# Kernel tuning notes

Measured on AMD Instinct MI355X. Metric: run time of the kernel, lower is better.

The kernel has to match this reference:

```python
import jax, jax.numpy as jnp
import numpy as np

D_MODEL = 768
D_STATE = 64
EXPAND = 2
D_INNER = EXPAND * D_MODEL
B, L = 2, 1024


def setup_inputs() -> dict:
    key = jax.random.key(0)
    ks = jax.random.split(key, 12)
    def xavier(k, shape):
        fan_in, fan_out = shape[0], shape[1]
        a = np.sqrt(6.0 / (fan_in + fan_out)).astype(np.float32)
        return jax.random.uniform(k, shape, jnp.float32, -a, a)
    x = jax.random.normal(ks[0], (B, L, D_MODEL), jnp.float32)
    W_in = xavier(ks[1], (D_MODEL, 2 * D_INNER))
    W_x = xavier(ks[2], (D_INNER, 2 * D_STATE + D_INNER))
    W_dt = xavier(ks[3], (D_STATE, D_INNER))
    b_dt = jax.random.uniform(ks[4], (D_INNER,), jnp.float32, -0.1, 0.1)
    A_log = jax.random.uniform(ks[5], (D_INNER, D_STATE), jnp.float32, -4.0, -1.0)
    Dp = 1.0 + 0.1 * jax.random.normal(ks[6], (D_INNER,), jnp.float32)
    W_out = xavier(ks[7], (D_INNER, D_MODEL))
    ln_g = jnp.ones((D_MODEL,), jnp.float32)
    ln_b = jnp.zeros((D_MODEL,), jnp.float32)
    return {"x": x, "W_in": W_in, "W_x": W_x, "W_dt": W_dt, "b_dt": b_dt,
            "A_log": A_log, "Dp": Dp, "W_out": W_out, "ln_g": ln_g, "ln_b": ln_b}


def _s6_forward(x, W_in, W_x, W_dt, b_dt, A_log, Dp, W_out, ln_g, ln_b):
    residual = x
    xr = x @ W_in                                    # (B,L,2*d_inner)
    xs, res = xr[..., :D_INNER], xr[..., D_INNER:]
    xs = jax.nn.silu(xs)
    # selective scan parameters
    x_dbl = xs @ W_x                                 # (B,L,2*d_state+d_inner)
    B_sel = x_dbl[..., :D_STATE]                     # (B,L,d_state)
    delta_in = x_dbl[..., D_STATE:2 * D_STATE]       # (B,L,d_state)
    C_sel = x_dbl[..., 2 * D_STATE:]                 # (B,L,d_inner)
    delta = jax.nn.softplus(delta_in @ W_dt + b_dt)  # (B,L,d_inner)
    delta = jnp.minimum(delta, 10.0)
    A = -jnp.exp(A_log.astype(jnp.float32))          # (d_inner,d_state)

    def step(h, inp):
        x_t, d_t, B_t, C_t = inp                     # (B,di) (B,di) (B,ds) (B,di)
        dA = jnp.exp(d_t[:, :, None] * A[None])      # (B,di,ds)
        dB = d_t[:, :, None] * B_t[:, None, :]       # (B,di,ds)
        h = dA * h + dB * x_t[:, :, None]
        y_t = C_t * jnp.sum(h, axis=-1)              # (B,di): sum(C[...,None]*h,-1)
        return h, y_t

    h0 = jnp.zeros((x.shape[0], D_INNER, D_STATE), xs.dtype)
    time_major = lambda a: jnp.swapaxes(a, 0, 1)
    _, ys = jax.lax.scan(step, h0, (time_major(xs), time_major(delta),
                                    time_major(B_sel), time_major(C_sel)))
    y = jnp.swapaxes(ys, 0, 1)                       # (B,L,d_inner)
    y = y + xs * Dp
    y = y * jax.nn.silu(res)
    out = y @ W_out + residual
    mu = jnp.mean(out, axis=-1, keepdims=True)
    var = jnp.var(out, axis=-1, keepdims=True)
    return (out - mu) * jax.lax.rsqrt(var + 1e-5) * ln_g + ln_b


def reference(x, W_in, W_x, W_dt, b_dt, A_log, Dp, W_out, ln_g, ln_b):
    return _s6_forward(x, W_in, W_x, W_dt, b_dt, A_log, Dp, W_out, ln_g, ln_b)
```

## Files before the change

kernel.cpp:

```cpp
#include <hip/hip_runtime.h>

typedef __bf16 bf16x8 __attribute__((ext_vector_type(8)));
typedef short short8 __attribute__((ext_vector_type(8)));
typedef float f32x4 __attribute__((ext_vector_type(4)));
typedef unsigned short ushort_t;

__device__ __forceinline__ ushort_t f2bf(float f) {
  union { float f; unsigned u; } v; v.f = f;
  unsigned r = v.u + 0x7fffu + ((v.u >> 16) & 1u);
  return (ushort_t)(r >> 16);
}
__device__ __forceinline__ float bf2f(ushort_t u) {
  return __int_as_float(((unsigned)u) << 16);
}

__device__ __forceinline__ void g2lds16(const void* g, void* l) {
  __builtin_amdgcn_global_load_lds(
      (const __attribute__((address_space(1))) void*)g,
      (__attribute__((address_space(3))) void*)l, 16, 0, 0);
}

__device__ __forceinline__ float rlane(float v, int l) {
  return __int_as_float(__builtin_amdgcn_readlane(__float_as_int(v), l));
}

__device__ __forceinline__ float fexp2(float x) {
#if __has_builtin(__builtin_amdgcn_exp2f)
  return __builtin_amdgcn_exp2f(x);
#else
  return exp2f(x);
#endif
}

template<int CTRL>
__device__ __forceinline__ float dpp_step(float x) {
  int t = __builtin_amdgcn_update_dpp(0, __float_as_int(x), CTRL, 0xf, 0xf, false);
  return x + __int_as_float(t);
}
__device__ __forceinline__ float wave_sum64(float v) {
  v = dpp_step<0x111>(v);
  v = dpp_step<0x112>(v);
  v = dpp_step<0x114>(v);
  v = dpp_step<0x118>(v);
  v = dpp_step<0x142>(v);
  v = dpp_step<0x143>(v);
  return v;
}
__device__ __forceinline__ float row_sum16(float v) {
  v = dpp_step<0x111>(v);
  v = dpp_step<0x112>(v);
  v = dpp_step<0x114>(v);
  v = dpp_step<0x118>(v);
  return v;
}
__device__ __forceinline__ float bcast_row15(float v) {
  return __int_as_float(__builtin_amdgcn_ds_swizzle(__float_as_int(v), 0x1F0));
}

__global__ __launch_bounds__(256)
void prep_kernel(const float* __restrict__ x, ushort_t* __restrict__ xbf,
                 const float* __restrict__ W_in, ushort_t* __restrict__ WinT,
                 const float* __restrict__ W_x, ushort_t* __restrict__ WxT,
                 const float* __restrict__ W_out, ushort_t* __restrict__ WoutT) {
  __shared__ float tile[32][33];
  const int r = blockIdx.x, tid = threadIdx.x;
  if (r < 1536) {
    int i = (r * 256 + tid) * 4;
    float4 v = *(const float4*)(x + i);
    union { ushort_t u[4]; uint2 v2; } o;
    o.u[0] = f2bf(v.x); o.u[1] = f2bf(v.y); o.u[2] = f2bf(v.z); o.u[3] = f2bf(v.w);
    *(uint2*)(xbf + i) = o.v2;
    return;
  }
  const float* W; ushort_t* Wt; int K, N, bx, by;
  if (r < 3840)      { int rr = r - 1536; W = W_in;  Wt = WinT;  K = 768;  N = 3072; bx = rr % 96; by = rr / 96; }
  else if (r < 6336) { int rr = r - 3840; W = W_x;   Wt = WxT;   K = 1536; N = 1664; bx = rr % 52; by = rr / 52; }
  else               { int rr = r - 6336; W = W_out; Wt = WoutT; K = 1536; N = 768;  bx = rr % 24; by = rr / 24; }
  const int n0 = bx * 32, k0 = by * 32;
  const int tx = tid & 31, ty = tid >> 5;
#pragma unroll
  for (int rr = 0; rr < 32; rr += 8)
    tile[ty + rr][tx] = W[(size_t)(k0 + ty + rr) * N + n0 + tx];
  __syncthreads();
#pragma unroll
  for (int rr = 0; rr < 32; rr += 8)
    Wt[(size_t)(n0 + ty + rr) * K + k0 + tx] = f2bf(tile[tx][ty + rr]);
}

template<int MODE>
__global__ __launch_bounds__(256)
void gemm_bf16(const ushort_t* __restrict__ A, const ushort_t* __restrict__ Bt,
               const int K, float* __restrict__ out0, ushort_t* __restrict__ out1,
               float* __restrict__ out2, const float* __restrict__ resid) {
  __shared__ __align__(16) ushort_t Asl[128 * 32];
  __shared__ __align__(16) ushort_t Bsl[128 * 32];
  const int tid = threadIdx.x;
  const int lane = tid & 63;
  const int wid = tid >> 6;
  const int wm = wid >> 1, wn = wid & 1;
  const int lr = lane & 15, lk = lane >> 4;
  const int bm = blockIdx.y, bn = blockIdx.x;
  const ushort_t* Ab = A + (size_t)bm * 128 * K;
  const ushort_t* Bb = Bt + (size_t)bn * 128 * K;

  f32x4 acc[4][4];
#pragma unroll
  for (int i = 0; i < 4; ++i)
#pragma unroll
    for (int j = 0; j < 4; ++j) acc[i][j] = (f32x4){0.f, 0.f, 0.f, 0.f};

  for (int k0 = 0; k0 < K; k0 += 32) {
#pragma unroll
    for (int it = 0; it < 2; ++it) {
      const int cb = ((it << 2) + wid) << 6;
      const int ch = cb + lane;
      const int row = ch >> 2;
      const int c8 = (ch & 3) << 3;
      g2lds16(Ab + (size_t)row * K + k0 + c8, Asl + (size_t)cb * 8);
      g2lds16(Bb + (size_t)row * K + k0 + c8, Bsl + (size_t)cb * 8);
    }
    __syncthreads();
    short8 av[4], bv[4];
#pragma unroll
    for (int i = 0; i < 4; ++i)
      av[i] = *(const short8*)(Asl + ((wm * 64 + i * 16 + lr) * 32 + lk * 8));
#pragma unroll
    for (int j = 0; j < 4; ++j)
      bv[j] = *(const short8*)(Bsl + ((wn * 64 + j * 16 + lr) * 32 + lk * 8));
#pragma unroll
    for (int i = 0; i < 4; ++i)
#pragma unroll
      for (int j = 0; j < 4; ++j)
        acc[i][j] = __builtin_amdgcn_mfma_f32_16x16x32_bf16(
            __builtin_bit_cast(bf16x8, av[i]), __builtin_bit_cast(bf16x8, bv[j]),
            acc[i][j], 0, 0, 0);
    __syncthreads();
  }

  const int mb = bm * 128 + wm * 64 + (lane >> 4) * 4;
  const int nb = bn * 128 + wn * 64 + (lane & 15);
#pragma unroll
  for (int i = 0; i < 4; ++i) {
#pragma unroll
    for (int j = 0; j < 4; ++j) {
      const int n = nb + j * 16;
#pragma unroll
      for (int r = 0; r < 4; ++r) {
        const int m = mb + i * 16 + r;
        float v = acc[i][j][r];
        if (MODE == 0) {
          float sv = v / (1.f + __expf(-v));
          if (n < 1536) {
            out0[(size_t)m * 1536 + n] = sv;
            out1[(size_t)m * 1536 + n] = f2bf(sv);
          } else {
            out2[(size_t)m * 1536 + (n - 1536)] = sv;
          }
        } else if (MODE == 1) {
          out0[(size_t)m * 1664 + n] = v;
        } else {
          const size_t id = (size_t)m * 768 + n;
          out0[id] = v + resid[id];
        }
      }
    }
  }
}

__global__ __launch_bounds__(256)
void dt_gemm(const float* __restrict__ xdbl, const float* __restrict__ Wdt,
             const float* __restrict__ bdt, float* __restrict__ delta) {
  __shared__ float Wl[64][256];
  __shared__ float Xl[32][64];
  const int tid = threadIdx.x;
  const int n0 = blockIdx.x << 8;
  const int m0 = blockIdx.y << 5;
  for (int i = tid; i < 64 * 256; i += 256) {
    int k = i >> 8, nn = i & 255;
    Wl[k][nn] = Wdt[(size_t)k * 1536 + n0 + nn];
  }
  for (int i = tid; i < 32 * 64; i += 256) {
    int mm = i >> 6, k = i & 63;
    Xl[mm][k] = xdbl[(size_t)(m0 + mm) * 1664 + 64 + k];
  }
  __syncthreads();
  float bv = bdt[n0 + tid];
  for (int mm = 0; mm < 32; ++mm) {
    float acc = bv;
#pragma unroll
    for (int k = 0; k < 64; ++k) acc = fmaf(Xl[mm][k], Wl[k][tid], acc);
    float sp = fmaxf(acc, 0.f) + log1pf(__expf(-fabsf(acc)));
    delta[(size_t)(m0 + mm) * 1536 + n0 + tid] = fminf(sp, 10.f);
  }
}


__global__ __launch_bounds__(256, 4)
void scan_pass1(const float* __restrict__ xdbl, const float* __restrict__ delta,
                const float* __restrict__ xs, const float* __restrict__ A_log,
                float* __restrict__ Qb, float* __restrict__ Dsum) {
  __shared__ __align__(16) ushort_t Btl[64 * 64];
  __shared__ __align__(16) float2 dtdx[64][16];
  const int tid = threadIdx.x;
  const int lane = tid & 63;
  const int wid = tid >> 6;
  const int i16 = lane & 15;
  const int ch = wid * 4 + (lane >> 4);
  const int seg = blockIdx.x, b = blockIdx.z;
  const int d0 = blockIdx.y * 16;
  const int d = d0 + ch;
  const int t0 = seg << 6;
  const size_t r0 = (size_t)b * 1024;

#pragma unroll
  for (int i = 0; i < 4; ++i) {
    int q = i * 256 + tid;
    int t = q >> 4, s0 = (q & 15) << 2;
    float4 v = *(const float4*)(xdbl + (r0 + t0 + t) * 1664 + s0);
    ushort4 u;
    u.x = f2bf(v.x); u.y = f2bf(v.y); u.z = f2bf(v.z); u.w = f2bf(v.w);
    *(ushort4*)&Btl[t * 64 + s0] = u;
  }
  float dtg[4];
#pragma unroll
  for (int c = 0; c < 4; ++c) {
    int dc = d0 + wid * 4 + c;
    dtg[c] = delta[(r0 + t0 + lane) * 1536 + dc];
    float dxg = dtg[c] * xs[(r0 + t0 + lane) * 1536 + dc];
    dtdx[lane][(wid * 4 + c) ^ i16] = make_float2(dtg[c], dxg);
  }
  float ds0 = rlane(wave_sum64(dtg[0]), 63);
  float ds1 = rlane(wave_sum64(dtg[1]), 63);
  float ds2 = rlane(wave_sum64(dtg[2]), 63);
  float ds3 = rlane(wave_sum64(dtg[3]), 63);
  if (lane == 0) {
    const size_t sb0 = (size_t)(b * 16 + seg) * 1536 + d0 + wid * 4;
    *(float4*)(Dsum + sb0) = make_float4(ds0, ds1, ds2, ds3);
  }

  float4 Av = *(const float4*)(A_log + (size_t)d * 64 + i16 * 4);
  const float A0 = -__expf(Av.x) * 1.44269504f;
  const float A1 = -__expf(Av.y) * 1.44269504f;
  const float A2 = -__expf(Av.z) * 1.44269504f;
  const float A3 = -__expf(Av.w) * 1.44269504f;

  __syncthreads();

  const ushort_t* Brow = Btl + (i16 << 2);
  float h0 = 0.f, h1 = 0.f, h2 = 0.f, h3 = 0.f;
#pragma unroll
  for (int tt = 0; tt < 64; ++tt) {
    float2 dd = dtdx[tt][ch ^ (tt & 15)];
    ushort4 ub = *(const ushort4*)(Brow + tt * 64);
    float dA0 = fexp2(dd.x * A0), dA1 = fexp2(dd.x * A1);
    float dA2 = fexp2(dd.x * A2), dA3 = fexp2(dd.x * A3);
    h0 = fmaf(dA0, h0, dd.y * bf2f(ub.x));
    h1 = fmaf(dA1, h1, dd.y * bf2f(ub.y));
    h2 = fmaf(dA2, h2, dd.y * bf2f(ub.z));
    h3 = fmaf(dA3, h3, dd.y * bf2f(ub.w));
  }
  const size_t sb = (size_t)(b * 16 + seg) * 1536 + d;
  *(float4*)(Qb + sb * 64 + i16 * 4) = make_float4(h0, h1, h2, h3);
}

__global__ __launch_bounds__(256, 4)
void scan_combine(float* __restrict__ Qb, const float* __restrict__ Dsum,
                  const float* __restrict__ A_log) {
  const int tid = threadIdx.x;
  const int lane = tid & 63;
  const int wave = blockIdx.x * 4 + (tid >> 6);
  const int bb = (wave >= 1536) ? 1 : 0;
  const int d = wave - bb * 1536;
  const float Aval2 = -__expf(A_log[(size_t)d * 64 + lane]) * 1.44269504f;
  float h = 0.f;
#pragma unroll
  for (int j = 0; j < 16; ++j) {
    const size_t sb = ((size_t)(bb * 16 + j) * 1536 + d);
    float q = Qb[sb * 64 + lane];
    float P = fexp2(Aval2 * Dsum[sb]);
    Qb[sb * 64 + lane] = h;
    h = fmaf(P, h, q);
  }
}

__global__ __launch_bounds__(256, 4)
void scan_pass2(const float* __restrict__ xdbl, const float* __restrict__ delta,
                const float* __restrict__ xs, const float* __restrict__ sres,
                const float* __restrict__ A_log, const float* __restrict__ Dp,
                const float* __restrict__ Qb, ushort_t* __restrict__ ybf) {
  __shared__ __align__(16) ushort_t Btl[64 * 64];
  __shared__ __align__(16) float2 dtdx[64][16];
  __shared__ __align__(16) float ytmp[64][16];
  const int tid = threadIdx.x;
  const int lane = tid & 63;
  const int wid = tid >> 6;
  const int i16 = lane & 15;
  const int ch = wid * 4 + (lane >> 4);
  const int seg = blockIdx.x, b = blockIdx.z;
  const int d0 = blockIdx.y * 16;
  const int d = d0 + ch;
  const int t0 = seg << 6;
  const size_t r0 = (size_t)b * 1024;

#pragma unroll
  for (int i = 0; i < 4; ++i) {
    int q = i * 256 + tid;
    int t = q >> 4, s0 = (q & 15) << 2;
    float4 v = *(const float4*)(xdbl + (r0 + t0 + t) * 1664 + s0);
    ushort4 u;
    u.x = f2bf(v.x); u.y = f2bf(v.y); u.z = f2bf(v.z); u.w = f2bf(v.w);
    *(ushort4*)&Btl[t * 64 + s0] = u;
  }
#pragma unroll
  for (int c = 0; c < 4; ++c) {
    int dc = d0 + wid * 4 + c;
    float dt = delta[(r0 + t0 + lane) * 1536 + dc];
    float dx = dt * xs[(r0 + t0 + lane) * 1536 + dc];
    dtdx[lane][(wid * 4 + c) ^ i16] = make_float2(dt, dx);
  }

  float4 Av = *(const float4*)(A_log + (size_t)d * 64 + i16 * 4);
  const float A0 = -__expf(Av.x) * 1.44269504f;
  const float A1 = -__expf(Av.y) * 1.44269504f;
  const float A2 = -__expf(Av.z) * 1.44269504f;
  const float A3 = -__expf(Av.w) * 1.44269504f;
  const size_t sb = (size_t)(b * 16 + seg) * 1536 + d;
  float4 hq = *(const float4*)(Qb + sb * 64 + i16 * 4);
  float h0 = hq.x, h1 = hq.y, h2 = hq.z, h3 = hq.w;

  __syncthreads();

  const ushort_t* Brow = Btl + (i16 << 2);
  float acc0 = 0.f, acc1 = 0.f, acc2 = 0.f, acc3 = 0.f;
#pragma unroll
  for (int tt = 0; tt < 64; ++tt) {
    float2 dd = dtdx[tt][ch ^ (tt & 15)];
    ushort4 ub = *(const ushort4*)(Brow + tt * 64);
    float dA0 = fexp2(dd.x * A0), dA1 = fexp2(dd.x * A1);
    float dA2 = fexp2(dd.x * A2), dA3 = fexp2(dd.x * A3);
    h0 = fmaf(dA0, h0, dd.y * bf2f(ub.x));
    h1 = fmaf(dA1, h1, dd.y * bf2f(ub.y));
    h2 = fmaf(dA2, h2, dd.y * bf2f(ub.z));
    h3 = fmaf(dA3, h3, dd.y * bf2f(ub.w));
    float s4 = (h0 + h1) + (h2 + h3);
    float Sv = bcast_row15(row_sum16(s4));
    bool m = (i16 == (tt & 15));
    if ((tt >> 4) == 0) acc0 = m ? Sv : acc0;
    else if ((tt >> 4) == 1) acc1 = m ? Sv : acc1;
    else if ((tt >> 4) == 2) acc2 = m ? Sv : acc2;
    else acc3 = m ? Sv : acc3;
  }

  ytmp[0 * 16 + i16][ch] = acc0;
  ytmp[1 * 16 + i16][ch] = acc1;
  ytmp[2 * 16 + i16][ch] = acc2;
  ytmp[3 * 16 + i16][ch] = acc3;
  __syncthreads();

  const int ch2 = tid & 15;
  const int tr = tid >> 4;
  const float dp2 = Dp[d0 + ch2];
#pragma unroll
  for (int r2 = 0; r2 < 4; ++r2) {
    const int t = tr + (r2 << 4);
    const size_t gi = r0 + t0 + t;
    float yv = ytmp[t][ch2];
    float Ct = xdbl[gi * 1664 + 128 + d0 + ch2];
    float xt = xs[gi * 1536 + d0 + ch2];
    float rt = sres[gi * 1536 + d0 + ch2];
    ybf[gi * 1536 + d0 + ch2] = f2bf((Ct * yv + xt * dp2) * rt);
  }
}

__global__ __launch_bounds__(256)
void ln_kernel(const float* __restrict__ in, const float* __restrict__ g,
               const float* __restrict__ be, float* __restrict__ outp) {
  const int row = blockIdx.x, tid = threadIdx.x;
  const float* p = in + (size_t)row * 768;
  float v0 = p[tid], v1 = p[tid + 256], v2 = p[tid + 512];
  __shared__ float sb[4];
  const int wid = tid >> 6;
  float s = wave_sum64(v0 + v1 + v2);
  if ((tid & 63) == 63) sb[wid] = s;
  __syncthreads();
  float mu = (sb[0] + sb[1] + sb[2] + sb[3]) * (1.f / 768.f);
  __syncthreads();
  float d0 = v0 - mu, d1 = v1 - mu, d2 = v2 - mu;
  float q = wave_sum64(d0 * d0 + d1 * d1 + d2 * d2);
  if ((tid & 63) == 63) sb[wid] = q;
  __syncthreads();
  float var = (sb[0] + sb[1] + sb[2] + sb[3]) * (1.f / 768.f);
  float inv = rsqrtf(var + 1e-5f);
  float* po = outp + (size_t)row * 768;
  po[tid]       = d0 * inv * g[tid]       + be[tid];
  po[tid + 256] = d1 * inv * g[tid + 256] + be[tid + 256];
  po[tid + 512] = d2 * inv * g[tid + 512] + be[tid + 512];
}

extern "C" void kernel_launch(void* const* d_in, const int* in_sizes, int n_in,
                              void* d_out, int out_size, void* d_ws, size_t ws_size,
                              hipStream_t stream) {
  (void)in_sizes; (void)n_in; (void)out_size; (void)ws_size;
  const float* x     = (const float*)d_in[0];
  const float* W_in  = (const float*)d_in[1];
  const float* W_x   = (const float*)d_in[2];
  const float* W_dt  = (const float*)d_in[3];
  const float* b_dt  = (const float*)d_in[4];
  const float* A_log = (const float*)d_in[5];
  const float* Dp    = (const float*)d_in[6];
  const float* W_out = (const float*)d_in[7];
  const float* ln_g  = (const float*)d_in[8];
  const float* ln_b  = (const float*)d_in[9];
  float* out = (float*)d_out;
  char* ws = (char*)d_ws;

  ushort_t* xbf   = (ushort_t*)(ws + 0);
  ushort_t* WinT  = (ushort_t*)(ws + 3145728);
  ushort_t* WxT   = (ushort_t*)(ws + 7864320);
  ushort_t* WoutT = (ushort_t*)(ws + 12976128);
  float*    xs_f  = (float*)   (ws + 15335424);
  ushort_t* xs_bf = (ushort_t*)(ws + 27918336);
  float*    sresp = (float*)   (ws + 34209792);
  float*    xdbl  = (float*)   (ws + 46792704);
  float*    dlt   = (float*)   (ws + 60424192);
  ushort_t* ybf   = (ushort_t*)(ws + 73007104);
  float*    otmp  = (float*)   (ws + 79298560);
  float*    Qbuf  = (float*)   (ws + 0);
  float*    Dsum  = (float*)   (ws + 12582912);

  prep_kernel<<<7488, 256, 0, stream>>>(x, xbf, W_in, WinT, W_x, WxT, W_out, WoutT);

  gemm_bf16<0><<<dim3(24, 16), 256, 0, stream>>>(xbf, WinT, 768, xs_f, xs_bf, sresp, nullptr);
  gemm_bf16<1><<<dim3(13, 16), 256, 0, stream>>>(xs_bf, WxT, 1536, xdbl, nullptr, nullptr, nullptr);
  dt_gemm<<<dim3(6, 64), 256, 0, stream>>>(xdbl, W_dt, b_dt, dlt);

  scan_pass1<<<dim3(16, 96, 2), 256, 0, stream>>>(xdbl, dlt, xs_f, A_log, Qbuf, Dsum);
  scan_combine<<<768, 256, 0, stream>>>(Qbuf, Dsum, A_log);
  scan_pass2<<<dim3(16, 96, 2), 256, 0, stream>>>(xdbl, dlt, xs_f, sresp, A_log, Dp, Qbuf, ybf);

  gemm_bf16<2><<<dim3(6, 16), 256, 0, stream>>>(ybf, WoutT, 1536, otmp, nullptr, nullptr, x);
  ln_kernel<<<2048, 256, 0, stream>>>(otmp, ln_g, ln_b, out);
}
```

Measured before the change: 236.7 us.

## Split-K the output GEMM four ways and fuse partial reduction into LayerNorm

The output projection GEMM previously launched only 96 blocks. It now splits K=1536 into four 384-wide slices via blockIdx.z and writes four fp32 partial outputs. The LayerNorm kernel sums the four partials plus the residual before normalizing, so the residual add moves out of the GEMM epilogue. This raises block count to fill the GPU, at the cost of extra partial-buffer write and read traffic. Min-occupancy hints were also dropped from the scan kernels' launch bounds.

```diff
diff --git a/kernel.cpp b/kernel.cpp
--- a/kernel.cpp
+++ b/kernel.cpp
@@ -90,7 +90,8 @@
 template<int MODE>
 __global__ __launch_bounds__(256)
 void gemm_bf16(const ushort_t* __restrict__ A, const ushort_t* __restrict__ Bt,
-               const int K, float* __restrict__ out0, ushort_t* __restrict__ out1,
+               const int K, const int lda, const int ldb,
+               float* __restrict__ out0, ushort_t* __restrict__ out1,
                float* __restrict__ out2, const float* __restrict__ resid) {
   __shared__ __align__(16) ushort_t Asl[128 * 32];
   __shared__ __align__(16) ushort_t Bsl[128 * 32];
@@ -100,8 +101,14 @@
   const int wm = wid >> 1, wn = wid & 1;
   const int lr = lane & 15, lk = lane >> 4;
   const int bm = blockIdx.y, bn = blockIdx.x;
-  const ushort_t* Ab = A + (size_t)bm * 128 * K;
-  const ushort_t* Bb = Bt + (size_t)bn * 128 * K;
+  if (MODE == 2) {
+    const int z = blockIdx.z;
+    A += z * 384;
+    Bt += z * 384;
+    out0 += (size_t)z * 2048 * 768;
+  }
+  const ushort_t* Ab = A + (size_t)bm * 128 * lda;
+  const ushort_t* Bb = Bt + (size_t)bn * 128 * ldb;
 
   f32x4 acc[4][4];
 #pragma unroll
@@ -116,8 +123,8 @@
       const int ch = cb + lane;
       const int row = ch >> 2;
       const int c8 = (ch & 3) << 3;
-      g2lds16(Ab + (size_t)row * K + k0 + c8, Asl + (size_t)cb * 8);
-      g2lds16(Bb + (size_t)row * K + k0 + c8, Bsl + (size_t)cb * 8);
+      g2lds16(Ab + (size_t)row * lda + k0 + c8, Asl + (size_t)cb * 8);
+      g2lds16(Bb + (size_t)row * ldb + k0 + c8, Bsl + (size_t)cb * 8);
     }
     __syncthreads();
     short8 av[4], bv[4];
@@ -159,8 +166,7 @@
         } else if (MODE == 1) {
           out0[(size_t)m * 1664 + n] = v;
         } else {
-          const size_t id = (size_t)m * 768 + n;
-          out0[id] = v + resid[id];
+          out0[(size_t)m * 768 + n] = v;
         }
       }
     }
@@ -195,7 +201,7 @@
 }
 
 
-__global__ __launch_bounds__(256, 4)
+__global__ __launch_bounds__(256)
 void scan_pass1(const float* __restrict__ xdbl, const float* __restrict__ delta,
                 const float* __restrict__ xs, const float* __restrict__ A_log,
                 float* __restrict__ Qb, float* __restrict__ Dsum) {
@@ -263,7 +269,7 @@
   *(float4*)(Qb + sb * 64 + i16 * 4) = make_float4(h0, h1, h2, h3);
 }
 
-__global__ __launch_bounds__(256, 4)
+__global__ __launch_bounds__(256)
 void scan_combine(float* __restrict__ Qb, const float* __restrict__ Dsum,
                   const float* __restrict__ A_log) {
   const int tid = threadIdx.x;
@@ -283,7 +289,7 @@
   }
 }
 
-__global__ __launch_bounds__(256, 4)
+__global__ __launch_bounds__(256)
 void scan_pass2(const float* __restrict__ xdbl, const float* __restrict__ delta,
                 const float* __restrict__ xs, const float* __restrict__ sres,
                 const float* __restrict__ A_log, const float* __restrict__ Dp,
@@ -373,11 +379,19 @@
 }
 
 __global__ __launch_bounds__(256)
-void ln_kernel(const float* __restrict__ in, const float* __restrict__ g,
-               const float* __restrict__ be, float* __restrict__ outp) {
+void ln_kernel(const float* __restrict__ part, const float* __restrict__ x,
+               const float* __restrict__ g, const float* __restrict__ be,
+               float* __restrict__ outp) {
   const int row = blockIdx.x, tid = threadIdx.x;
-  const float* p = in + (size_t)row * 768;
-  float v0 = p[tid], v1 = p[tid + 256], v2 = p[tid + 512];
+  const size_t ro = (size_t)row * 768;
+  const float* p0 = part + ro;
+  const float* p1 = part + 1572864 + ro;
+  const float* p2 = part + 3145728 + ro;
+  const float* p3 = part + 4718592 + ro;
+  const float* xr = x + ro;
+  float v0 = p0[tid] + p1[tid] + p2[tid] + p3[tid] + xr[tid];
+  float v1 = p0[tid + 256] + p1[tid + 256] + p2[tid + 256] + p3[tid + 256] + xr[tid + 256];
+  float v2 = p0[tid + 512] + p1[tid + 512] + p2[tid + 512] + p3[tid + 512] + xr[tid + 512];
   __shared__ float sb[4];
   const int wid = tid >> 6;
   float s = wave_sum64(v0 + v1 + v2);
@@ -391,7 +405,7 @@
   __syncthreads();
   float var = (sb[0] + sb[1] + sb[2] + sb[3]) * (1.f / 768.f);
   float inv = rsqrtf(var + 1e-5f);
-  float* po = outp + (size_t)row * 768;
+  float* po = outp + ro;
   po[tid]       = d0 * inv * g[tid]       + be[tid];
   po[tid + 256] = d1 * inv * g[tid + 256] + be[tid + 256];
   po[tid + 512] = d2 * inv * g[tid + 512] + be[tid + 512];
@@ -424,20 +438,23 @@
   float*    xdbl  = (float*)   (ws + 46792704);
   float*    dlt   = (float*)   (ws + 60424192);
   ushort_t* ybf   = (ushort_t*)(ws + 73007104);
-  float*    otmp  = (float*)   (ws + 79298560);
   float*    Qbuf  = (float*)   (ws + 0);
   float*    Dsum  = (float*)   (ws + 12582912);
+  float*    part  = (float*)   (ws + 15335424);
 
   prep_kernel<<<7488, 256, 0, stream>>>(x, xbf, W_in, WinT, W_x, WxT, W_out, WoutT);
 
-  gemm_bf16<0><<<dim3(24, 16), 256, 0, stream>>>(xbf, WinT, 768, xs_f, xs_bf, sresp, nullptr);
-  gemm_bf16<1><<<dim3(13, 16), 256, 0, stream>>>(xs_bf, WxT, 1536, xdbl, nullptr, nullptr, nullptr);
+  gemm_bf16<0><<<dim3(24, 16), 256, 0, stream>>>(xbf, WinT, 768, 768, 768,
+                                                 xs_f, xs_bf, sresp, nullptr);
+  gemm_bf16<1><<<dim3(13, 16), 256, 0, stream>>>(xs_bf, WxT, 1536, 1536, 1536,
+                                                 xdbl, nullptr, nullptr, nullptr);
   dt_gemm<<<dim3(6, 64), 256, 0, stream>>>(xdbl, W_dt, b_dt, dlt);
 
   scan_pass1<<<dim3(16, 96, 2), 256, 0, stream>>>(xdbl, dlt, xs_f, A_log, Qbuf, Dsum);
   scan_combine<<<768, 256, 0, stream>>>(Qbuf, Dsum, A_log);
   scan_pass2<<<dim3(16, 96, 2), 256, 0, stream>>>(xdbl, dlt, xs_f, sresp, A_log, Dp, Qbuf, ybf);
 
-  gemm_bf16<2><<<dim3(6, 16), 256, 0, stream>>>(ybf, WoutT, 1536, otmp, nullptr, nullptr, x);
-  ln_kernel<<<2048, 256, 0, stream>>>(otmp, ln_g, ln_b, out);
-}
+  gemm_bf16<2><<<dim3(6, 16, 4), 256, 0, stream>>>(ybf, WoutT, 384, 1536, 1536,
+                                                   part, nullptr, nullptr, nullptr);
+  ln_kernel<<<2048, 256, 0, stream>>>(part, x, ln_g, ln_b, out);
+}
```

Result: faster. 219.2 us (-7.4%).
